# Kernel tuning notes

Measured on AMD Instinct MI355X. Metric: run time of the kernel, lower is better.

## Reference

```python
import jax, jax.numpy as jnp
import numpy as np


def _deform_unfold(feat, offset):
    """Deformable 3x3 unfold with bilinear sampling, zero padding outside.
    feat: [B,C,H,W], offset: [B,2K,H,W] (y,x per point). Returns [B,C,K,H,W]."""
    B, C, H, W = feat.shape
    K = offset.shape[1] // 2
    off = offset.reshape(B, K, 2, H, W)
    # 3x3 kernel grid, dilation 1, padding 1 -> relative taps in {-1,0,1}
    ky = (jnp.arange(K) // 3 - 1).astype(feat.dtype)
    kx = (jnp.arange(K) % 3 - 1).astype(feat.dtype)
    hh = jnp.arange(H, dtype=feat.dtype)
    ww = jnp.arange(W, dtype=feat.dtype)
    py = hh[None, None, :, None] + ky[None, :, None, None] + off[:, :, 0]  # [B,K,H,W]
    px = ww[None, None, None, :] + kx[None, :, None, None] + off[:, :, 1]  # [B,K,H,W]
    y0 = jnp.floor(py)
    x0 = jnp.floor(px)
    fy = py - y0  # frac weights
    fx = px - x0
    y0i = y0.astype(jnp.int32)
    x0i = x0.astype(jnp.int32)

    def gather(yi, xi):
        valid = ((yi >= 0) & (yi < H) & (xi >= 0) & (xi < W)).astype(feat.dtype)
        yc = jnp.clip(yi, 0, H - 1)
        xc = jnp.clip(xi, 0, W - 1)
        v = jax.vmap(lambda f, yy, xx: f[:, yy, xx])(feat, yc, xc)  # [B,C,K,H,W]
        return v * valid[:, None]

    w00 = ((1 - fy) * (1 - fx))[:, None]
    w01 = ((1 - fy) * fx)[:, None]
    w10 = (fy * (1 - fx))[:, None]
    w11 = (fy * fx)[:, None]
    return (gather(y0i, x0i) * w00 + gather(y0i, x0i + 1) * w01 +
            gather(y0i + 1, x0i) * w10 + gather(y0i + 1, x0i + 1) * w11)


def setup_inputs() -> dict:
    key = jax.random.key(0)
    ks = jax.random.split(key, 8)
    B, C, H, W = 4, 256, 64, 64
    Ci, P = 128, 9
    x = jax.random.normal(ks[0], (B, C, H, W), jnp.float32)
    offset = jax.random.normal(ks[1], (B, 2 * P, H, W), jnp.float32)
    std = 0.01  # normal_init(std=0.01)
    Wq = jax.random.normal(ks[2], (Ci, C), jnp.float32) * std
    Wk = jax.random.normal(ks[3], (Ci, C), jnp.float32) * std
    Wv = jax.random.normal(ks[4], (Ci, C), jnp.float32) * std
    Wo = jax.random.normal(ks[5], (Ci,), jnp.float32) * std
    bq = jnp.zeros((Ci,), jnp.float32)
    bk = jnp.zeros((Ci,), jnp.float32)
    bv = jnp.zeros((Ci,), jnp.float32)
    bo = jnp.zeros((1,), jnp.float32)
    return {"x": x, "offset": offset, "Wq": Wq, "bq": bq, "Wk": Wk, "bk": bk,
            "Wv": Wv, "bv": bv, "Wo": Wo, "bo": bo}


def reference(x, offset, Wq, bq, Wk, bk, Wv, bv, Wo, bo):
    # 1x1 conv projections
    q = jnp.einsum('bchw,oc->bohw', x, Wq) + bq[None, :, None, None]
    k = jnp.einsum('bchw,oc->bohw', x, Wk) + bk[None, :, None, None]
    v = jnp.einsum('bchw,oc->bohw', x, Wv) + bv[None, :, None, None]
    qu = _deform_unfold(q, offset)  # [B,Ci,K,H,W]
    ku = _deform_unfold(k, offset)  # [B,Ci,K,H,W]
    vu = _deform_unfold(v, offset)  # [B,Ci,K,H,W]
    # per-pixel KxK attention: query [K,Ci] @ key [Ci,K]
    scores = jnp.einsum('bcihw,bcjhw->bijhw', qu, ku)  # [B,K,K,H,W]
    attn = jax.nn.softmax(scores, axis=2)
    # attn [K,K] @ value [K,Ci]
    out_v = jnp.einsum('bijhw,bcjhw->bcihw', attn, vu)  # [B,Ci,K,H,W]
    # conv_out: 1x1 conv Ci->1 over the value, then sigmoid -> [B,K,H,W]
    out = jnp.einsum('bcihw,c->bihw', out_v, Wo) + bo[0]
    return jax.nn.sigmoid(out)
```

## Files before the change

kernel.cpp:

```cpp
#include <hip/hip_runtime.h>

typedef unsigned short u16;
typedef unsigned int u32;

#define B_   4
#define C_   256
#define CI_  128
#define H_   64
#define W_   64
#define NPB_ 4096
#define NP_  16384
#define K_   9
#define MROWS_ 272

typedef __attribute__((ext_vector_type(8))) __bf16 bf16x8_t;
typedef __attribute__((ext_vector_type(4))) float f32x4_t;
typedef __attribute__((ext_vector_type(2))) float f32x2_t;

__device__ __forceinline__ float bf2f(u16 u) {
    union { u32 i; float f; } x; x.i = ((u32)u) << 16; return x.f;
}
__device__ __forceinline__ float bf2f_lo(u32 w) {
    union { u32 i; float f; } x; x.i = w << 16; return x.f;
}
__device__ __forceinline__ float bf2f_hi(u32 w) {
    union { u32 i; float f; } x; x.i = w & 0xffff0000u; return x.f;
}
__device__ __forceinline__ u16 f2bf(float f) {
    union { float f; u32 i; } x; x.f = f;
    u32 lsb = (x.i >> 16) & 1u;
    return (u16)((x.i + 0x7fffu + lsb) >> 16);
}
__device__ __forceinline__ void acc8p(f32x2_t* f, uint4 v, f32x2_t w2) {
    f32x2_t p;
    p.x = bf2f_lo(v.x); p.y = bf2f_hi(v.x); f[0] += w2 * p;
    p.x = bf2f_lo(v.y); p.y = bf2f_hi(v.y); f[1] += w2 * p;
    p.x = bf2f_lo(v.z); p.y = bf2f_hi(v.z); f[2] += w2 * p;
    p.x = bf2f_lo(v.w); p.y = bf2f_hi(v.w); f[3] += w2 * p;
}

__global__ void k0b_prep(const float* __restrict__ Wq, const float* __restrict__ bq,
                         const float* __restrict__ Wk, const float* __restrict__ bk,
                         const float* __restrict__ Wv, const float* __restrict__ bv,
                         const float* __restrict__ Wo,
                         u16* __restrict__ Wbf, float* __restrict__ bias) {
    const int o = blockIdx.x;
    const int c = threadIdx.x;
    if (o < 128) {
        Wbf[o * C_ + c] = f2bf(Wq[o * C_ + c]);
        if (c == 0) bias[o] = bq[o];
    } else if (o < 256) {
        Wbf[o * C_ + c] = f2bf(Wk[(o - 128) * C_ + c]);
        if (c == 0) bias[o] = bk[o - 128];
    } else if (o == 256) {
        float s = 0.f;
        #pragma unroll 8
        for (int oo = 0; oo < CI_; ++oo)
            s += Wo[oo] * Wv[oo * C_ + c];
        Wbf[o * C_ + c] = f2bf(s);
        if (c == 0) {
            float ts = 0.f;
            #pragma unroll 8
            for (int oo = 0; oo < CI_; ++oo) ts += Wo[oo] * bv[oo];
            bias[256] = ts;
        }
    } else {
        Wbf[o * C_ + c] = 0;
        if (c == 0) bias[o] = 0.f;
    }
}

__global__ __launch_bounds__(512) void k1_proj(
    const float* __restrict__ x, const u16* __restrict__ Wbf,
    const float* __restrict__ bias,
    u16* __restrict__ qk, float* __restrict__ vs) {
    __shared__ u16 xs[16][264];
    const int t = threadIdx.x;
    const int l = t & 63;
    const int w = t >> 6;
    const int lane16 = l & 15;
    const int g = l >> 4;
    const int p0 = blockIdx.x * 16;
    const int b = p0 >> 12;
    const int pin = p0 & 4095;
    const int px = p0 + lane16;

    {
        const int c = t >> 1;
        const int ph = (t & 1) * 8;
        const float* src = x + (size_t)(b * C_ + c) * NPB_ + pin + ph;
        const float4 v0 = *reinterpret_cast<const float4*>(src);
        const float4 v1 = *reinterpret_cast<const float4*>(src + 4);
        xs[ph + 0][c] = f2bf(v0.x); xs[ph + 1][c] = f2bf(v0.y);
        xs[ph + 2][c] = f2bf(v0.z); xs[ph + 3][c] = f2bf(v0.w);
        xs[ph + 4][c] = f2bf(v1.x); xs[ph + 5][c] = f2bf(v1.y);
        xs[ph + 6][c] = f2bf(v1.z); xs[ph + 7][c] = f2bf(v1.w);
    }
    __syncthreads();

    const int mt0 = 2 * w;
    const int nmt = (w < 7) ? 2 : 3;

    f32x4_t acc[3];
    #pragma unroll
    for (int n = 0; n < 3; ++n) {
        const int mt = mt0 + n;
        #pragma unroll
        for (int r = 0; r < 4; ++r)
            acc[n][r] = (n < nmt) ? bias[mt * 16 + g * 4 + r] : 0.f;
    }

    #pragma unroll
    for (int kk = 0; kk < 8; ++kk) {
        const int c0 = kk * 32 + g * 8;
        const bf16x8_t bv = *reinterpret_cast<const bf16x8_t*>(&xs[lane16][c0]);
        const u16* arow = Wbf + c0 + (size_t)(mt0 * 16 + lane16) * C_;
        #pragma unroll
        for (int n = 0; n < 3; ++n) {
            if (n < nmt) {
                const bf16x8_t av = *reinterpret_cast<const bf16x8_t*>(arow + (size_t)n * 16 * C_);
                acc[n] = __builtin_amdgcn_mfma_f32_16x16x32_bf16(av, bv, acc[n], 0, 0, 0);
            }
        }
    }

    u16* qrow = qk + (size_t)px * C_;
    #pragma unroll
    for (int n = 0; n < 3; ++n) {
        const int mt = mt0 + n;
        if (n < nmt && mt < 16) {
            u32* dst = reinterpret_cast<u32*>(qrow + mt * 16 + g * 4);
            dst[0] = (u32)f2bf(acc[n][0]) | ((u32)f2bf(acc[n][1]) << 16);
            dst[1] = (u32)f2bf(acc[n][2]) | ((u32)f2bf(acc[n][3]) << 16);
        }
    }
    if (w == 7 && g == 0) vs[px] = acc[2][0];
}

__global__ __launch_bounds__(256) void k2_attn(
    const float* __restrict__ off, const u16* __restrict__ qk,
    const float* __restrict__ vs, const float* __restrict__ bo,
    float* __restrict__ out) {
    const int t = threadIdx.x;
    const int l = t & 63;
    const int bid = blockIdx.x;
    const int swz = (bid & 7) * ((int)gridDim.x >> 3) + (bid >> 3);
    const int pixel = swz * 4 + (t >> 6);
    const int b = pixel >> 12;
    const int rem = pixel & 4095;
    const int y = rem >> 6, xx = rem & 63;
    const int l16 = l & 15;
    const int tap = (l16 < K_) ? l16 : (K_ - 1);
    const int g = l >> 4;

    const float* offb = off + ((size_t)b * (2 * K_) + 2 * tap) * NPB_ + rem;
    const float oy = offb[0];
    const float ox = offb[NPB_];
    const float py = (float)(y + tap / 3 - 1) + oy;
    const float px = (float)(xx + tap % 3 - 1) + ox;
    const float fy0 = floorf(py), fx0 = floorf(px);
    const float fy = py - fy0, fx = px - fx0;
    const int y0 = (int)fy0, x0 = (int)fx0;

    const u16* qkb = qk + ((size_t)(b << 12)) * C_ + g * 8;
    const float* vsm = vs + (b << 12);

    float wgt[4];
    int ppc[4];
    const u16* bp[4];
    #pragma unroll
    for (int c = 0; c < 4; ++c) {
        const int dy = c >> 1, dx = c & 1;
        const int yi = y0 + dy, xi = x0 + dx;
        const float wv = (dy ? fy : 1.f - fy) * (dx ? fx : 1.f - fx);
        const int ok = (yi >= 0) & (yi < H_) & (xi >= 0) & (xi < W_);
        const int yc = min(max(yi, 0), H_ - 1);
        const int xc = min(max(xi, 0), W_ - 1);
        ppc[c] = yc * W_ + xc;
        wgt[c] = ok ? wv : 0.f;
        bp[c] = qkb + (size_t)ppc[c] * C_;
    }

    uint4 qv[4][4], kv[4][4];
    #pragma unroll
    for (int c = 0; c < 4; ++c) {
        #pragma unroll
        for (int s = 0; s < 4; ++s) {
            qv[c][s] = *reinterpret_cast<const uint4*>(bp[c] + s * 32);
            kv[c][s] = *reinterpret_cast<const uint4*>(bp[c] + CI_ + s * 32);
        }
    }
    const float vsu_t = wgt[0] * vsm[ppc[0]] + wgt[1] * vsm[ppc[1]] +
                        wgt[2] * vsm[ppc[2]] + wgt[3] * vsm[ppc[3]];

    f32x2_t fq[16], fk[16];
    #pragma unroll
    for (int e = 0; e < 16; ++e) { fq[e] = (f32x2_t){0.f, 0.f}; fk[e] = (f32x2_t){0.f, 0.f}; }
    #pragma unroll
    for (int s = 0; s < 4; ++s) {
        #pragma unroll
        for (int c = 0; c < 4; ++c) {
            const f32x2_t w2 = {wgt[c], wgt[c]};
            acc8p(&fq[s * 4], qv[c][s], w2);
            acc8p(&fk[s * 4], kv[c][s], w2);
        }
    }

    f32x4_t acc = {0.f, 0.f, 0.f, 0.f};
    #pragma unroll
    for (int s = 0; s < 4; ++s) {
        bf16x8_t av, bv;
        #pragma unroll
        for (int e = 0; e < 4; ++e) {
            av[2 * e]     = (__bf16)fk[s * 4 + e].x;
            av[2 * e + 1] = (__bf16)fk[s * 4 + e].y;
            bv[2 * e]     = (__bf16)fq[s * 4 + e].x;
            bv[2 * e + 1] = (__bf16)fq[s * 4 + e].y;
        }
        acc = __builtin_amdgcn_mfma_f32_16x16x32_bf16(av, bv, acc, 0, 0, 0);
    }

    float mx = -1e30f;
    #pragma unroll
    for (int r = 0; r < 4; ++r) {
        const int j = g * 4 + r;
        if (j < K_) mx = fmaxf(mx, acc[r]);
    }
    mx = fmaxf(mx, __shfl_xor(mx, 16, 64));
    mx = fmaxf(mx, __shfl_xor(mx, 32, 64));

    float vj[4];
    #pragma unroll
    for (int r = 0; r < 4; ++r) vj[r] = __shfl(vsu_t, g * 4 + r, 64);

    float den = 0.f, num = 0.f;
    #pragma unroll
    for (int r = 0; r < 4; ++r) {
        const int j = g * 4 + r;
        if (j < K_) {
            const float e = __expf(acc[r] - mx);
            den += e;
            num += e * vj[r];
        }
    }
    den += __shfl_xor(den, 16, 64); den += __shfl_xor(den, 32, 64);
    num += __shfl_xor(num, 16, 64); num += __shfl_xor(num, 32, 64);

    if (l < K_) {
        const float z = num / den + bo[0];
        out[(size_t)b * K_ * NPB_ + (size_t)l * NPB_ + rem] = 1.f / (1.f + __expf(-z));
    }
}

extern "C" void kernel_launch(void* const* d_in, const int* in_sizes, int n_in,
                              void* d_out, int out_size, void* d_ws, size_t ws_size,
                              hipStream_t stream) {
    const float* x   = (const float*)d_in[0];
    const float* off = (const float*)d_in[1];
    const float* Wq  = (const float*)d_in[2];
    const float* bq  = (const float*)d_in[3];
    const float* Wk  = (const float*)d_in[4];
    const float* bk  = (const float*)d_in[5];
    const float* Wv  = (const float*)d_in[6];
    const float* bv  = (const float*)d_in[7];
    const float* Wo  = (const float*)d_in[8];
    const float* bo  = (const float*)d_in[9];
    float* out = (float*)d_out;

    char* ws = (char*)d_ws;
    u16*   qkbuf = (u16*)(ws + 4096);
    float* vsmap = (float*)(ws + 4096 + 8388608);
    u16*   Wbf   = (u16*)(ws + 4096 + 8388608 + 65536);
    float* bias  = (float*)(ws + 4096 + 8388608 + 65536 + 139264);

    k0b_prep<<<MROWS_, 256, 0, stream>>>(Wq, bq, Wk, bk, Wv, bv, Wo, Wbf, bias);
    k1_proj<<<NP_ / 16, 512, 0, stream>>>(x, Wbf, bias, qkbuf, vsmap);
    k2_attn<<<NP_ / 4, 256, 0, stream>>>(off, qkbuf, vsmap, bo, out);
}
```

Measured before the change: 78.06 us.

## Pre-swizzle projection weights into MFMA fragment layout and vectorize x staging

The prep kernel now writes bf16 weights in a tiled layout so that each lane's MFMA A-operand is one contiguous 16-byte load. The previous row-strided loads needed several cache lines per wave. The x tile is staged into LDS with one packed 16-byte store per thread instead of scattered 2-byte stores. Every wave now also computes the vsum tile (tile 16) redundantly, which removes the uneven 2-vs-3 tile split and its branches. The attention kernel hoists its vsmap gathers behind a sched_barrier and sets launch_bounds(256,1), which may change register allocation and occupancy.

```diff
diff --git a/kernel.cpp b/kernel.cpp
--- a/kernel.cpp
+++ b/kernel.cpp
@@ -43,21 +43,22 @@
                          const float* __restrict__ Wk, const float* __restrict__ bk,
                          const float* __restrict__ Wv, const float* __restrict__ bv,
                          const float* __restrict__ Wo,
-                         u16* __restrict__ Wbf, float* __restrict__ bias) {
+                         u16* __restrict__ Wt, float* __restrict__ bias) {
     const int o = blockIdx.x;
     const int c = threadIdx.x;
+    u16 val;
     if (o < 128) {
-        Wbf[o * C_ + c] = f2bf(Wq[o * C_ + c]);
+        val = f2bf(Wq[o * C_ + c]);
         if (c == 0) bias[o] = bq[o];
     } else if (o < 256) {
-        Wbf[o * C_ + c] = f2bf(Wk[(o - 128) * C_ + c]);
+        val = f2bf(Wk[(o - 128) * C_ + c]);
         if (c == 0) bias[o] = bk[o - 128];
     } else if (o == 256) {
         float s = 0.f;
         #pragma unroll 8
         for (int oo = 0; oo < CI_; ++oo)
             s += Wo[oo] * Wv[oo * C_ + c];
-        Wbf[o * C_ + c] = f2bf(s);
+        val = f2bf(s);
         if (c == 0) {
             float ts = 0.f;
             #pragma unroll 8
@@ -65,16 +66,19 @@
             bias[256] = ts;
         }
     } else {
-        Wbf[o * C_ + c] = 0;
+        val = 0;
         if (c == 0) bias[o] = 0.f;
     }
+    const int mt = o >> 4, l16 = o & 15;
+    const int kk = c >> 5, g = (c >> 3) & 3, e = c & 7;
+    Wt[(size_t)((mt * 8 + kk) * 64 + g * 16 + l16) * 8 + e] = val;
 }
 
 __global__ __launch_bounds__(512) void k1_proj(
-    const float* __restrict__ x, const u16* __restrict__ Wbf,
+    const float* __restrict__ x, const u16* __restrict__ Wt,
     const float* __restrict__ bias,
     u16* __restrict__ qk, float* __restrict__ vs) {
-    __shared__ u16 xs[16][264];
+    __shared__ u16 xs[16][272];
     const int t = threadIdx.x;
     const int l = t & 63;
     const int w = t >> 6;
@@ -83,61 +87,54 @@
     const int p0 = blockIdx.x * 16;
     const int b = p0 >> 12;
     const int pin = p0 & 4095;
+
+    {
+        const int spx = t & 15, cg = t >> 4;
+        const float* src = x + (size_t)(b * C_ + cg * 8) * NPB_ + pin + spx;
+        float v[8];
+        #pragma unroll
+        for (int i = 0; i < 8; ++i) v[i] = src[(size_t)i * NPB_];
+        uint4 pk;
+        pk.x = (u32)f2bf(v[0]) | ((u32)f2bf(v[1]) << 16);
+        pk.y = (u32)f2bf(v[2]) | ((u32)f2bf(v[3]) << 16);
+        pk.z = (u32)f2bf(v[4]) | ((u32)f2bf(v[5]) << 16);
+        pk.w = (u32)f2bf(v[6]) | ((u32)f2bf(v[7]) << 16);
+        *reinterpret_cast<uint4*>(&xs[spx][cg * 8]) = pk;
+    }
+    __syncthreads();
+
+    const int mts[3] = {2 * w, 2 * w + 1, 16};
+    f32x4_t acc[3];
+    #pragma unroll
+    for (int n = 0; n < 3; ++n)
+        #pragma unroll
+        for (int r = 0; r < 4; ++r)
+            acc[n][r] = bias[mts[n] * 16 + g * 4 + r];
+
+    #pragma unroll
+    for (int kk = 0; kk < 8; ++kk) {
+        const bf16x8_t bv = *reinterpret_cast<const bf16x8_t*>(&xs[lane16][kk * 32 + g * 8]);
+        #pragma unroll
+        for (int n = 0; n < 3; ++n) {
+            const bf16x8_t av = *reinterpret_cast<const bf16x8_t*>(
+                Wt + (size_t)((mts[n] * 8 + kk) * 64 + l) * 8);
+            acc[n] = __builtin_amdgcn_mfma_f32_16x16x32_bf16(av, bv, acc[n], 0, 0, 0);
+        }
+    }
+
     const int px = p0 + lane16;
-
-    {
-        const int c = t >> 1;
-        const int ph = (t & 1) * 8;
-        const float* src = x + (size_t)(b * C_ + c) * NPB_ + pin + ph;
-        const float4 v0 = *reinterpret_cast<const float4*>(src);
-        const float4 v1 = *reinterpret_cast<const float4*>(src + 4);
-        xs[ph + 0][c] = f2bf(v0.x); xs[ph + 1][c] = f2bf(v0.y);
-        xs[ph + 2][c] = f2bf(v0.z); xs[ph + 3][c] = f2bf(v0.w);
-        xs[ph + 4][c] = f2bf(v1.x); xs[ph + 5][c] = f2bf(v1.y);
-        xs[ph + 6][c] = f2bf(v1.z); xs[ph + 7][c] = f2bf(v1.w);
-    }
-    __syncthreads();
-
-    const int mt0 = 2 * w;
-    const int nmt = (w < 7) ? 2 : 3;
-
-    f32x4_t acc[3];
-    #pragma unroll
-    for (int n = 0; n < 3; ++n) {
-        const int mt = mt0 + n;
-        #pragma unroll
-        for (int r = 0; r < 4; ++r)
-            acc[n][r] = (n < nmt) ? bias[mt * 16 + g * 4 + r] : 0.f;
-    }
-
-    #pragma unroll
-    for (int kk = 0; kk < 8; ++kk) {
-        const int c0 = kk * 32 + g * 8;
-        const bf16x8_t bv = *reinterpret_cast<const bf16x8_t*>(&xs[lane16][c0]);
-        const u16* arow = Wbf + c0 + (size_t)(mt0 * 16 + lane16) * C_;
-        #pragma unroll
-        for (int n = 0; n < 3; ++n) {
-            if (n < nmt) {
-                const bf16x8_t av = *reinterpret_cast<const bf16x8_t*>(arow + (size_t)n * 16 * C_);
-                acc[n] = __builtin_amdgcn_mfma_f32_16x16x32_bf16(av, bv, acc[n], 0, 0, 0);
-            }
-        }
-    }
-
     u16* qrow = qk + (size_t)px * C_;
     #pragma unroll
-    for (int n = 0; n < 3; ++n) {
-        const int mt = mt0 + n;
-        if (n < nmt && mt < 16) {
-            u32* dst = reinterpret_cast<u32*>(qrow + mt * 16 + g * 4);
-            dst[0] = (u32)f2bf(acc[n][0]) | ((u32)f2bf(acc[n][1]) << 16);
-            dst[1] = (u32)f2bf(acc[n][2]) | ((u32)f2bf(acc[n][3]) << 16);
-        }
-    }
-    if (w == 7 && g == 0) vs[px] = acc[2][0];
-}
-
-__global__ __launch_bounds__(256) void k2_attn(
+    for (int n = 0; n < 2; ++n) {
+        const int mt = mts[n];
+        u32* dst = reinterpret_cast<u32*>(qrow + mt * 16 + g * 4);
+        dst[0] = (u32)f2bf(acc[n][0]) | ((u32)f2bf(acc[n][1]) << 16);
+        dst[1] = (u32)f2bf(acc[n][2]) | ((u32)f2bf(acc[n][3]) << 16);
+    }
+    if (w == 0 && g == 0) vs[px] = acc[2][0];
+}
+
+__global__ __launch_bounds__(256, 1) void k2_attn(
     const float* __restrict__ off, const u16* __restrict__ qk,
     const float* __restrict__ vs, const float* __restrict__ bo,
     float* __restrict__ out) {
@@ -190,8 +187,13 @@
             kv[c][s] = *reinterpret_cast<const uint4*>(bp[c] + CI_ + s * 32);
         }
     }
-    const float vsu_t = wgt[0] * vsm[ppc[0]] + wgt[1] * vsm[ppc[1]] +
-                        wgt[2] * vsm[ppc[2]] + wgt[3] * vsm[ppc[3]];
+    float vsc[4];
+    #pragma unroll
+    for (int c = 0; c < 4; ++c) vsc[c] = vsm[ppc[c]];
+    __builtin_amdgcn_sched_barrier(0);
+
+    const float vsu_t = wgt[0] * vsc[0] + wgt[1] * vsc[1] +
+                        wgt[2] * vsc[2] + wgt[3] * vsc[3];
 
     f32x2_t fq[16], fk[16];
     #pragma unroll
@@ -270,10 +272,10 @@
     char* ws = (char*)d_ws;
     u16*   qkbuf = (u16*)(ws + 4096);
     float* vsmap = (float*)(ws + 4096 + 8388608);
-    u16*   Wbf   = (u16*)(ws + 4096 + 8388608 + 65536);
+    u16*   Wt    = (u16*)(ws + 4096 + 8388608 + 65536);
     float* bias  = (float*)(ws + 4096 + 8388608 + 65536 + 139264);
 
-    k0b_prep<<<MROWS_, 256, 0, stream>>>(Wq, bq, Wk, bk, Wv, bv, Wo, Wbf, bias);
-    k1_proj<<<NP_ / 16, 512, 0, stream>>>(x, Wbf, bias, qkbuf, vsmap);
+    k0b_prep<<<MROWS_, 256, 0, stream>>>(Wq, bq, Wk, bk, Wv, bv, Wo, Wt, bias);
+    k1_proj<<<NP_ / 16, 512, 0, stream>>>(x, Wt, bias, qkbuf, vsmap);
     k2_attn<<<NP_ / 4, 256, 0, stream>>>(off, qkbuf, vsmap, bo, out);
 }
```

New measurement: 76.93 us. No clear change (-1.5%).
